# Kernel optimization log

Measured on AMD Instinct MI355X. Metric: run time of the kernel, lower is better.

The kernel has to match this reference:

```python
import jax, jax.numpy as jnp
import numpy as np

B = 32
NODES = [20480, 5120, 1280, 320, 80]
K = 6
Z = 64


def _cheb_sparse(x, src, dst, norm, W, b):
    # x: [B, N, F]; Chebyshev recursion with sparse normalized adjacency (edge list)
    def prop(t):
        return jnp.zeros_like(t).at[:, dst, :].add(t[:, src, :] * norm[None, :, None])
    Tx0 = x
    out = jnp.einsum('bnf,fo->bno', Tx0, W[0])
    Tx1 = prop(x)
    out = out + jnp.einsum('bnf,fo->bno', Tx1, W[1])
    for k in range(2, W.shape[0]):
        Tx2 = 2.0 * prop(Tx1) - Tx0
        out = out + jnp.einsum('bnf,fo->bno', Tx2, W[k])
        Tx0, Tx1 = Tx1, Tx2
    return out if b is None else out + b


def _cheb_dense(x, adj, W, b):
    # x: [B, N, F]; adj: dense [N, N] (adjacency_matrices[i].to_dense())
    Tx0 = x
    out = jnp.einsum('bnf,fo->bno', Tx0, W[0])
    Tx1 = jnp.einsum('mn,bnf->bmf', adj, x)
    out = out + jnp.einsum('bnf,fo->bno', Tx1, W[1])
    for k in range(2, W.shape[0]):
        Tx2 = 2.0 * jnp.einsum('mn,bnf->bmf', adj, Tx1) - Tx0
        out = out + jnp.einsum('bnf,fo->bno', Tx2, W[k])
        Tx0, Tx1 = Tx1, Tx2
    return out if b is None else out + b


def _pool(x, idx, w):
    # sparse pooling matrix with <=3 nnz/row: out[b,m,f] = sum_k w[m,k] * x[b, idx[m,k], f]
    return jnp.einsum('mk,bmkf->bmf', w, x[:, idx, :])


def setup_inputs() -> dict:
    key = jax.random.key(0)
    ks = iter(jax.random.split(key, 96))
    N0 = NODES[0]
    E = N0 * 6
    inp = {}
    inp['x'] = jax.random.normal(next(ks), (B * N0, 3), jnp.float32)
    ei = jax.random.randint(next(ks), (2, E), 0, N0, jnp.int32)
    inp['edge_index0'] = ei
    src, dst = ei[0], ei[1]
    deg = jnp.zeros((N0,), jnp.float32).at[src].add(1.0)
    dinv = jnp.where(deg > 0, deg ** -0.5, 0.0)
    inp['A_norm0'] = dinv[src] * dinv[dst]
    inp['batch_size'] = B
    for i in (1, 2, 3):
        n = NODES[i]
        inp[f'adj{i}'] = jax.random.uniform(next(ks), (n, n), jnp.float32) / n
    for i in range(4):
        m, n = NODES[i + 1], NODES[i]
        inp[f'down_idx{i}'] = jax.random.randint(next(ks), (m, 3), 0, n, jnp.int32)
        inp[f'down_w{i}'] = jax.random.uniform(next(ks), (m, 3), jnp.float32) / 3.0
        inp[f'up_idx{i}'] = jax.random.randint(next(ks), (n, 3), 0, m, jnp.int32)
        inp[f'up_w{i}'] = jax.random.uniform(next(ks), (n, 3), jnp.float32) / 3.0
    enc_io = [(3, 16), (16, 16), (16, 16), (16, 32)]
    for i, (fi, fo) in enumerate(enc_io):
        inp[f'W_enc{i}'] = 0.1 * jax.random.normal(next(ks), (K, fi, fo), jnp.float32)
        inp[f'b_enc{i}'] = 0.1 * jax.random.normal(next(ks), (fo,), jnp.float32)
    dec_io = [(32, 16), (16, 16), (16, 16), (16, 16), (16, 3)]
    for i, (fi, fo) in enumerate(dec_io):
        inp[f'W_dec{i}'] = 0.1 * jax.random.normal(next(ks), (K, fi, fo), jnp.float32)
        if i < 4:
            inp[f'b_dec{i}'] = 0.1 * jax.random.normal(next(ks), (fo,), jnp.float32)
    lat_in = NODES[4] * 32  # 2560
    inp['enc_w'] = 0.1 * jax.random.normal(next(ks), (Z, lat_in), jnp.float32)
    inp['enc_b'] = 0.1 * jax.random.normal(next(ks), (Z,), jnp.float32)
    inp['dec_w'] = 0.1 * jax.random.normal(next(ks), (lat_in, Z), jnp.float32)
    inp['dec_b'] = 0.1 * jax.random.normal(next(ks), (lat_in,), jnp.float32)
    return inp


def reference(x, edge_index0, A_norm0, batch_size, adj1, adj2, adj3,
              down_idx0, down_w0, up_idx0, up_w0, down_idx1, down_w1, up_idx1, up_w1,
              down_idx2, down_w2, up_idx2, up_w2, down_idx3, down_w3, up_idx3, up_w3,
              W_enc0, b_enc0, W_enc1, b_enc1, W_enc2, b_enc2, W_enc3, b_enc3,
              W_dec0, b_dec0, W_dec1, b_dec1, W_dec2, b_dec2, W_dec3, b_dec3, W_dec4,
              enc_w, enc_b, dec_w, dec_b):
    relu = jax.nn.relu
    src, dst = edge_index0[0], edge_index0[1]
    h = x.reshape(batch_size, -1, x.shape[-1])
    # encoder
    h = relu(_cheb_sparse(h, src, dst, A_norm0, W_enc0, b_enc0)); h = _pool(h, down_idx0, down_w0)
    h = relu(_cheb_dense(h, adj1, W_enc1, b_enc1)); h = _pool(h, down_idx1, down_w1)
    h = relu(_cheb_dense(h, adj2, W_enc2, b_enc2)); h = _pool(h, down_idx2, down_w2)
    h = relu(_cheb_dense(h, adj3, W_enc3, b_enc3)); h = _pool(h, down_idx3, down_w3)
    z = relu(h.reshape(batch_size, -1) @ enc_w.T + enc_b)
    # decoder
    h = relu(z @ dec_w.T + dec_b).reshape(batch_size, -1, W_dec0.shape[1])
    h = _pool(h, up_idx3, up_w3); h = relu(_cheb_dense(h, adj3, W_dec0, b_dec0))
    h = _pool(h, up_idx2, up_w2); h = relu(_cheb_dense(h, adj2, W_dec1, b_dec1))
    h = _pool(h, up_idx1, up_w1); h = relu(_cheb_dense(h, adj1, W_dec2, b_dec2))
    h = _pool(h, up_idx0, up_w0); h = relu(_cheb_sparse(h, src, dst, A_norm0, W_dec3, b_dec3))
    h = _cheb_sparse(h, src, dst, A_norm0, W_dec4, None)  # final layer, bias=None
    return h.reshape(-1, x.shape[-1])
```

## Files before the change

kernel.cpp:

```cpp
#include <hip/hip_runtime.h>

#define BATCH 32
#define NN0   20480

typedef __attribute__((ext_vector_type(8))) short short8v;
typedef __attribute__((ext_vector_type(4))) float f32x4;

__device__ __forceinline__ float bf2f(unsigned short h) {
    return __uint_as_float(((unsigned int)h) << 16);
}
__device__ __forceinline__ unsigned short f2bf(float x) {
    unsigned int u = __float_as_uint(x);
    u += 0x7fff + ((u >> 16) & 1);
    return (unsigned short)(u >> 16);
}
__device__ __forceinline__ unsigned int pk2(float a, float b) {
    return (unsigned int)f2bf(a) | ((unsigned int)f2bf(b) << 16);
}

__global__ __launch_bounds__(256) void count_kernel(const int* __restrict__ dst, int* __restrict__ cnt, int E) {
    int e = blockIdx.x * 256 + threadIdx.x;
    if (e < E) atomicAdd(&cnt[dst[e]], 1);
}

__global__ __launch_bounds__(256) void scan_kernel(const int* __restrict__ cnt, int* __restrict__ rowptr,
                                                   int* __restrict__ cursor, int n) {
    __shared__ int part[256];
    int tid = threadIdx.x;
    int per = (n + 255) / 256;
    int start = tid * per;
    int end = start + per; if (end > n) end = n; if (start > n) start = n;
    int s = 0;
    for (int i = start; i < end; ++i) s += cnt[i];
    part[tid] = s;
    __syncthreads();
    for (int off = 1; off < 256; off <<= 1) {
        int v = (tid >= off) ? part[tid - off] : 0;
        __syncthreads();
        part[tid] += v;
        __syncthreads();
    }
    int base = (tid == 0) ? 0 : part[tid - 1];
    for (int i = start; i < end; ++i) {
        rowptr[i] = base; cursor[i] = base;
        base += cnt[i];
    }
    if (tid == 255) rowptr[n] = base;
}

__global__ __launch_bounds__(256) void scatter_kernel(const int* __restrict__ src, const int* __restrict__ dst,
                                                      const float* __restrict__ nrm, int* __restrict__ cursor,
                                                      int* __restrict__ esrc, float* __restrict__ ewt,
                                                      int* __restrict__ eid, int E) {
    int e = blockIdx.x * 256 + threadIdx.x;
    if (e >= E) return;
    int p = atomicAdd(&cursor[dst[e]], 1);
    esrc[p] = src[e]; ewt[p] = nrm[e]; eid[p] = e;
}

__global__ __launch_bounds__(256) void sortrows_kernel(const int* __restrict__ rowptr, int* __restrict__ esrc,
                                                       float* __restrict__ ewt, int* __restrict__ eid, int N) {
    int m = blockIdx.x * 256 + threadIdx.x;
    if (m >= N) return;
    int a = rowptr[m], b = rowptr[m + 1];
    for (int i = a + 1; i < b; ++i) {
        int ke = eid[i]; int ks = esrc[i]; float kw = ewt[i];
        int j = i - 1;
        while (j >= a && eid[j] > ke) { eid[j+1]=eid[j]; esrc[j+1]=esrc[j]; ewt[j+1]=ewt[j]; --j; }
        eid[j+1] = ke; esrc[j+1] = ks; ewt[j+1] = kw;
    }
}

__global__ __launch_bounds__(256) void convert_flat(const float* __restrict__ in, unsigned short* __restrict__ out,
                                                    size_t n4) {
    for (size_t i = blockIdx.x * 256 + threadIdx.x; i < n4; i += (size_t)gridDim.x * 256) {
        float4 v = reinterpret_cast<const float4*>(in)[i];
        ushort4 o;
        o.x = f2bf(v.x); o.y = f2bf(v.y); o.z = f2bf(v.z); o.w = f2bf(v.w);
        reinterpret_cast<ushort4*>(out)[i] = o;
    }
}

__global__ __launch_bounds__(256) void xcopy_T(const float* __restrict__ x, unsigned short* __restrict__ out) {
    __shared__ unsigned short sh[32 * 96];
    const int m0 = blockIdx.x * 32;
    const int tid = threadIdx.x;
    const int b = tid >> 3, mi = tid & 7;
#pragma unroll
    for (int ii = 0; ii < 4; ++ii) {
        int mm = mi + ii * 8;
        const float* p = x + ((size_t)b * NN0 + m0 + mm) * 3;
        sh[mm * 96 + b * 3 + 0] = f2bf(p[0]);
        sh[mm * 96 + b * 3 + 1] = f2bf(p[1]);
        sh[mm * 96 + b * 3 + 2] = f2bf(p[2]);
    }
    __syncthreads();
    unsigned int* dst = (unsigned int*)(out + (size_t)m0 * 96);
    const unsigned int* srcp = (const unsigned int*)sh;
    for (int i = tid; i < 32 * 48; i += 256) dst[i] = srcp[i];
}

__global__ __launch_bounds__(256) void sparse_prop16(const int* __restrict__ rowptr, const int* __restrict__ esrc,
                                                     const float* __restrict__ ewt,
                                                     const unsigned short* __restrict__ Tin,
                                                     const unsigned short* __restrict__ Tprev,
                                                     unsigned short* __restrict__ Tout, float s, float t) {
    int g = blockIdx.x * 256 + threadIdx.x;
    int m = g >> 6, lane = g & 63;
    int e0 = rowptr[m], e1 = rowptr[m + 1];
    float acc[8] = {};
    for (int e = e0; e < e1; ++e) {
        float w = ewt[e];
        short8v v = *reinterpret_cast<const short8v*>(Tin + (size_t)esrc[e] * 512 + lane * 8);
#pragma unroll
        for (int j = 0; j < 8; ++j) acc[j] += w * bf2f((unsigned short)v[j]);
    }
    float r[8];
    if (Tprev) {
        short8v pv = *reinterpret_cast<const short8v*>(Tprev + (size_t)m * 512 + lane * 8);
#pragma unroll
        for (int j = 0; j < 8; ++j) r[j] = s * acc[j] + t * bf2f((unsigned short)pv[j]);
    } else {
#pragma unroll
        for (int j = 0; j < 8; ++j) r[j] = s * acc[j];
    }
    uint4 ov;
    ov.x = pk2(r[0], r[1]); ov.y = pk2(r[2], r[3]); ov.z = pk2(r[4], r[5]); ov.w = pk2(r[6], r[7]);
    *reinterpret_cast<uint4*>(Tout + (size_t)m * 512 + lane * 8) = ov;
}

__global__ __launch_bounds__(256) void sparse_prop3(const int* __restrict__ rowptr, const int* __restrict__ esrc,
                                                    const float* __restrict__ ewt,
                                                    const unsigned short* __restrict__ Tin,
                                                    const unsigned short* __restrict__ Tprev,
                                                    unsigned short* __restrict__ Tout, float s, float t) {
    int g = blockIdx.x * 256 + threadIdx.x;
    int m = g / 96, c = g - m * 96;
    int e0 = rowptr[m], e1 = rowptr[m + 1];
    float acc = 0.f;
    for (int e = e0; e < e1; ++e)
        acc += ewt[e] * bf2f(Tin[(size_t)esrc[e] * 96 + c]);
    float v = s * acc;
    if (Tprev) v += t * bf2f(Tprev[(size_t)m * 96 + c]);
    Tout[(size_t)m * 96 + c] = f2bf(v);
}

template <int FIN, int FOUT>
__global__ __launch_bounds__(256) void sparse_epi(const unsigned short* __restrict__ S, size_t slot,
                                                  const float* __restrict__ W, const float* __restrict__ bias,
                                                  unsigned short* __restrict__ out, int relu) {
    __shared__ float Ws[6 * FIN * FOUT];
    for (int i = threadIdx.x; i < 6 * FIN * FOUT; i += 256) Ws[i] = W[i];
    __syncthreads();
    int g = blockIdx.x * 256 + threadIdx.x;
    int m = g >> 5, b = g & 31;
    float oa[FOUT];
#pragma unroll
    for (int o = 0; o < FOUT; ++o) oa[o] = bias ? bias[o] : 0.f;
    for (int k = 0; k < 6; ++k) {
        const unsigned short* p = S + (size_t)k * slot + (size_t)m * (32 * FIN) + b * FIN;
        float xv[FIN];
        if constexpr (FIN == 16) {
            short8v v0 = *reinterpret_cast<const short8v*>(p);
            short8v v1 = *reinterpret_cast<const short8v*>(p + 8);
#pragma unroll
            for (int f = 0; f < 8; ++f) { xv[f] = bf2f((unsigned short)v0[f]); xv[f + 8] = bf2f((unsigned short)v1[f]); }
        } else {
#pragma unroll
            for (int f = 0; f < FIN; ++f) xv[f] = bf2f(p[f]);
        }
#pragma unroll
        for (int f = 0; f < FIN; ++f)
#pragma unroll
            for (int o = 0; o < FOUT; ++o) oa[o] += xv[f] * Ws[(k * FIN + f) * FOUT + o];
    }
    unsigned short* orow = out + (size_t)m * (32 * FOUT) + b * FOUT;
    unsigned int u[FOUT / 2];
#pragma unroll
    for (int o = 0; o < FOUT / 2; ++o) {
        float a = oa[2 * o], c = oa[2 * o + 1];
        if (relu) { a = fmaxf(a, 0.f); c = fmaxf(c, 0.f); }
        u[o] = pk2(a, c);
    }
#pragma unroll
    for (int q = 0; q < FOUT / 8; ++q)
        reinterpret_cast<uint4*>(orow)[q] = make_uint4(u[4 * q], u[4 * q + 1], u[4 * q + 2], u[4 * q + 3]);
}

__global__ __launch_bounds__(256) void sparse_epi_final(const unsigned short* __restrict__ S, size_t slot,
                                                        const float* __restrict__ W, float* __restrict__ dout) {
    __shared__ float Ws[6 * 16 * 3];
    __shared__ float sh[32 * 24];
    for (int i = threadIdx.x; i < 288; i += 256) Ws[i] = W[i];
    __syncthreads();
    const int tid = threadIdx.x;
    const int mm = tid >> 5, b = tid & 31;
    const int m = blockIdx.x * 8 + mm;
    float o0 = 0.f, o1 = 0.f, o2 = 0.f;
    for (int k = 0; k < 6; ++k) {
        const unsigned short* p = S + (size_t)k * slot + (size_t)m * 512 + b * 16;
        short8v v0 = *reinterpret_cast<const short8v*>(p);
        short8v v1 = *reinterpret_cast<const short8v*>(p + 8);
#pragma unroll
        for (int f = 0; f < 16; ++f) {
            float xf = bf2f((unsigned short)(f < 8 ? v0[f] : v1[f - 8]));
            o0 += xf * Ws[(k * 16 + f) * 3 + 0];
            o1 += xf * Ws[(k * 16 + f) * 3 + 1];
            o2 += xf * Ws[(k * 16 + f) * 3 + 2];
        }
    }
    sh[b * 24 + mm * 3 + 0] = o0;
    sh[b * 24 + mm * 3 + 1] = o1;
    sh[b * 24 + mm * 3 + 2] = o2;
    __syncthreads();
    const size_t base = (size_t)blockIdx.x * 24;
    for (int i = tid; i < 768; i += 256) {
        int b2 = i / 24, r = i - b2 * 24;
        dout[(size_t)b2 * (NN0 * 3) + base + r] = sh[i];
    }
}

__device__ __forceinline__ float ldv(const float* p) { return *p; }
__device__ __forceinline__ float ldv(const unsigned short* p) { return bf2f(*p); }

template <typename TI>
__global__ __launch_bounds__(256) void pool_cT(const TI* __restrict__ in, const int* __restrict__ idx,
                                               const float* __restrict__ w, unsigned short* __restrict__ out,
                                               int C, int Mnew) {
    __shared__ float tile[32][33];
    const int m0 = blockIdx.x * 32, c0 = blockIdx.y * 32;
    const int tx = threadIdx.x & 31, ty = threadIdx.x >> 5;
#pragma unroll
    for (int i = 0; i < 4; ++i) {
        int mn = m0 + ty + i * 8;
        const int* ir = idx + mn * 3; const float* wr = w + mn * 3;
        float v = wr[0] * ldv(in + (size_t)ir[0] * C + c0 + tx)
                + wr[1] * ldv(in + (size_t)ir[1] * C + c0 + tx)
                + wr[2] * ldv(in + (size_t)ir[2] * C + c0 + tx);
        tile[ty + i * 8][tx] = v;
    }
    __syncthreads();
#pragma unroll
    for (int i = 0; i < 4; ++i) {
        int c = c0 + ty + i * 8;
        out[(size_t)c * Mnew + m0 + tx] = f2bf(tile[tx][ty + i * 8]);
    }
}

__global__ __launch_bounds__(256) void pool_row16(const unsigned short* __restrict__ in, const int* __restrict__ idx,
                                                  const float* __restrict__ w, unsigned short* __restrict__ out) {
    int g = blockIdx.x * 256 + threadIdx.x;
    int m = g >> 6, lane = g & 63;
    const int* ir = idx + m * 3; const float* wr = w + m * 3;
    short8v a = *reinterpret_cast<const short8v*>(in + (size_t)ir[0] * 512 + lane * 8);
    short8v b = *reinterpret_cast<const short8v*>(in + (size_t)ir[1] * 512 + lane * 8);
    short8v c = *reinterpret_cast<const short8v*>(in + (size_t)ir[2] * 512 + lane * 8);
    float r[8];
#pragma unroll
    for (int j = 0; j < 8; ++j)
        r[j] = wr[0] * bf2f((unsigned short)a[j]) + wr[1] * bf2f((unsigned short)b[j]) + wr[2] * bf2f((unsigned short)c[j]);
    uint4 ov;
    ov.x = pk2(r[0], r[1]); ov.y = pk2(r[2], r[3]); ov.z = pk2(r[4], r[5]); ov.w = pk2(r[6], r[7]);
    *reinterpret_cast<uint4*>(out + (size_t)m * 512 + lane * 8) = ov;
}

__global__ __launch_bounds__(256) void pool_f32(const unsigned short* __restrict__ in, const int* __restrict__ idx,
                                                const float* __restrict__ w, float* __restrict__ out) {
    int g = blockIdx.x * 256 + threadIdx.x;
    int m = g >> 10, c = g & 1023;
    const int* ir = idx + m * 3; const float* wr = w + m * 3;
    out[g] = wr[0] * bf2f(in[(size_t)ir[0] * 1024 + c])
           + wr[1] * bf2f(in[(size_t)ir[1] * 1024 + c])
           + wr[2] * bf2f(in[(size_t)ir[2] * 1024 + c]);
}

template <int MF, bool SPLIT>
__global__ __launch_bounds__(256) void gemm_mfma(const unsigned short* __restrict__ Ab,
                                                 const unsigned short* __restrict__ Xb,
                                                 const unsigned short* __restrict__ Pb,
                                                 unsigned short* __restrict__ Ob,
                                                 float* __restrict__ Pf,
                                                 int Mn, int KC, float s, float t) {
    constexpr int BM = MF * 64;
    __shared__ unsigned short As[BM * 64];
    __shared__ unsigned short Xs[64 * 64];
    const int tid = threadIdx.x;
    const int lane = tid & 63, wid = tid >> 6;
    int lin = blockIdx.y * gridDim.x + blockIdx.x;
    int nwg = gridDim.x * gridDim.y;
    int lin2 = (lin & 7) * (nwg >> 3) + (lin >> 3);
    int by = lin2 / gridDim.x, bx = lin2 - by * gridDim.x;
    const int bm = by * BM, bc = bx * 64;
    const int kbase = SPLIT ? blockIdx.z * KC : 0;

    f32x4 acc[MF][4] = {};
    constexpr int SEGA = (BM * 64 * 2) / 1024 / 4;

    for (int k0 = kbase; k0 < kbase + KC; k0 += 64) {
        __syncthreads();
#pragma unroll
        for (int i = 0; i < SEGA; ++i) {
            int o = (wid * SEGA + i) * 1024 + lane * 16;
            int row = o >> 7;
            int colb = (o & 127) ^ ((row & 7) << 4);
            const unsigned short* g = Ab + (size_t)(bm + row) * Mn + k0 + (colb >> 1);
            __builtin_amdgcn_global_load_lds((const __attribute__((address_space(1))) void*)g,
                                             (__attribute__((address_space(3))) void*)((char*)As + (size_t)(wid * SEGA + i) * 1024),
                                             16, 0, 0);
        }
#pragma unroll
        for (int i = 0; i < 2; ++i) {
            int o = (wid * 2 + i) * 1024 + lane * 16;
            int row = o >> 7;
            int colb = (o & 127) ^ ((row & 7) << 4);
            const unsigned short* g = Xb + (size_t)(bc + row) * Mn + k0 + (colb >> 1);
            __builtin_amdgcn_global_load_lds((const __attribute__((address_space(1))) void*)g,
                                             (__attribute__((address_space(3))) void*)((char*)Xs + (size_t)(wid * 2 + i) * 1024),
                                             16, 0, 0);
        }
        __syncthreads();
#pragma unroll
        for (int kk = 0; kk < 2; ++kk) {
            short8v a[MF], b[4];
#pragma unroll
            for (int mf = 0; mf < MF; ++mf) {
                int r = wid * (MF * 16) + mf * 16 + (lane & 15);
                int cb = kk * 64 + ((lane >> 4) * 16);
                int addr = r * 128 + (cb ^ ((r & 7) << 4));
                a[mf] = *reinterpret_cast<const short8v*>((const char*)As + addr);
            }
#pragma unroll
            for (int cf = 0; cf < 4; ++cf) {
                int r = cf * 16 + (lane & 15);
                int cb = kk * 64 + ((lane >> 4) * 16);
                int addr = r * 128 + (cb ^ ((r & 7) << 4));
                b[cf] = *reinterpret_cast<const short8v*>((const char*)Xs + addr);
            }
#pragma unroll
            for (int mf = 0; mf < MF; ++mf)
#pragma unroll
                for (int cf = 0; cf < 4; ++cf)
                    acc[mf][cf] = __builtin_amdgcn_mfma_f32_16x16x32_bf16(a[mf], b[cf], acc[mf][cf], 0, 0, 0);
        }
    }
#pragma unroll
    for (int mf = 0; mf < MF; ++mf) {
        int m0 = bm + wid * (MF * 16) + mf * 16 + ((lane >> 4) * 4);
#pragma unroll
        for (int cf = 0; cf < 4; ++cf) {
            int c = bc + cf * 16 + (lane & 15);
            size_t base = (size_t)c * Mn + m0;
            if constexpr (SPLIT) {
                size_t zbase = (size_t)blockIdx.z * (size_t)(gridDim.x * 64) * (size_t)Mn;
                *reinterpret_cast<float4*>(Pf + zbase + base) =
                    make_float4(acc[mf][cf][0], acc[mf][cf][1], acc[mf][cf][2], acc[mf][cf][3]);
            } else {
                float v0 = s * acc[mf][cf][0], v1 = s * acc[mf][cf][1];
                float v2 = s * acc[mf][cf][2], v3 = s * acc[mf][cf][3];
                if (Pb) {
                    uint2 pv = *reinterpret_cast<const uint2*>(Pb + base);
                    v0 += t * bf2f((unsigned short)(pv.x & 0xffff));
                    v1 += t * bf2f((unsigned short)(pv.x >> 16));
                    v2 += t * bf2f((unsigned short)(pv.y & 0xffff));
                    v3 += t * bf2f((unsigned short)(pv.y >> 16));
                }
                uint2 ov;
                ov.x = pk2(v0, v1); ov.y = pk2(v2, v3);
                *reinterpret_cast<uint2*>(Ob + base) = ov;
            }
        }
    }
}

__global__ __launch_bounds__(256) void sk_reduce(const float* __restrict__ Pf,
                                                 const unsigned short* __restrict__ Prev,
                                                 unsigned short* __restrict__ Out,
                                                 int n4, int KS, float s, float t) {
    int g = blockIdx.x * 256 + threadIdx.x;
    if (g >= n4) return;
    float4 a = reinterpret_cast<const float4*>(Pf)[g];
    for (int ks = 1; ks < KS; ++ks) {
        float4 b = reinterpret_cast<const float4*>(Pf)[(size_t)ks * n4 + g];
        a.x += b.x; a.y += b.y; a.z += b.z; a.w += b.w;
    }
    float v0 = s * a.x, v1 = s * a.y, v2 = s * a.z, v3 = s * a.w;
    if (Prev) {
        uint2 pv = reinterpret_cast<const uint2*>(Prev)[g];
        v0 += t * bf2f((unsigned short)(pv.x & 0xffff));
        v1 += t * bf2f((unsigned short)(pv.x >> 16));
        v2 += t * bf2f((unsigned short)(pv.y & 0xffff));
        v3 += t * bf2f((unsigned short)(pv.y >> 16));
    }
    uint2 ov;
    ov.x = pk2(v0, v1); ov.y = pk2(v2, v3);
    reinterpret_cast<uint2*>(Out)[g] = ov;
}

template <int FIN, int FOUT>
__global__ __launch_bounds__(256) void epi_layer(const unsigned short* __restrict__ Tb, size_t tslot,
                                                 const float* __restrict__ W, const float* __restrict__ bias,
                                                 unsigned short* __restrict__ out, int M) {
    __shared__ float Ws[6 * FIN * FOUT];
    for (int i = threadIdx.x; i < 6 * FIN * FOUT; i += 256) Ws[i] = W[i];
    __syncthreads();
    int g = blockIdx.x * 256 + threadIdx.x;
    int b = g / M, m = g - b * M;
    float oa[FOUT];
#pragma unroll
    for (int o = 0; o < FOUT; ++o) oa[o] = bias[o];
    for (int k = 0; k < 6; ++k) {
        const unsigned short* Tk = Tb + (size_t)k * tslot + (size_t)b * FIN * M + m;
#pragma unroll
        for (int f = 0; f < FIN; ++f) {
            float xf = bf2f(Tk[(size_t)f * M]);
#pragma unroll
            for (int o = 0; o < FOUT; ++o) oa[o] += xf * Ws[(k * FIN + f) * FOUT + o];
        }
    }
    unsigned short* orow = out + (size_t)m * (32 * FOUT) + b * FOUT;
    unsigned int u[FOUT / 2];
#pragma unroll
    for (int o = 0; o < FOUT / 2; ++o)
        u[o] = pk2(fmaxf(oa[2 * o], 0.f), fmaxf(oa[2 * o + 1], 0.f));
#pragma unroll
    for (int q = 0; q < FOUT / 8; ++q)
        reinterpret_cast<uint4*>(orow)[q] = make_uint4(u[4 * q], u[4 * q + 1], u[4 * q + 2], u[4 * q + 3]);
}

__global__ __launch_bounds__(256) void fc_enc_kernel(const float* __restrict__ h, const float* __restrict__ w,
                                                     const float* __restrict__ bias, float* __restrict__ z) {
    __shared__ float sh[256];
    int b = blockIdx.x, o = threadIdx.x & 63, q = threadIdx.x >> 6;
    float acc = 0.f;
    for (int n = q * 20; n < q * 20 + 20; ++n)
#pragma unroll
        for (int f = 0; f < 32; ++f)
            acc += h[((size_t)n * 32 + b) * 32 + f] * w[(size_t)o * 2560 + n * 32 + f];
    sh[threadIdx.x] = acc;
    __syncthreads();
    if (q == 0) z[b * 64 + o] = fmaxf(sh[o] + sh[64 + o] + sh[128 + o] + sh[192 + o] + bias[o], 0.f);
}

__global__ __launch_bounds__(256) void fc_dec_kernel(const float* __restrict__ z, const float* __restrict__ w,
                                                     const float* __restrict__ bias, float* __restrict__ out) {
    int g = blockIdx.x * 256 + threadIdx.x;
    if (g >= 80 * 32 * 32) return;
    int f = g % 32; int b = (g / 32) % 32; int n = g / 1024;
    int j = n * 32 + f;
    float acc = bias[j];
    const float* wr = w + (size_t)j * 64;
    const float* zr = z + b * 64;
#pragma unroll
    for (int o = 0; o < 64; ++o) acc += zr[o] * wr[o];
    out[g] = fmaxf(acc, 0.f);
}

extern "C" void kernel_launch(void* const* d_in, const int* in_sizes, int n_in,
                              void* d_out, int out_size, void* d_ws, size_t ws_size,
                              hipStream_t stream) {
    (void)n_in; (void)out_size; (void)ws_size;
    const float* x     = (const float*)d_in[0];
    const int*   ei    = (const int*)d_in[1];
    const float* anorm = (const float*)d_in[2];
    const float* adjs[3] = { (const float*)d_in[4], (const float*)d_in[5], (const float*)d_in[6] };
    const int*   dn_idx[4] = { (const int*)d_in[7],  (const int*)d_in[11], (const int*)d_in[15], (const int*)d_in[19] };
    const float* dn_w[4]   = { (const float*)d_in[8],(const float*)d_in[12],(const float*)d_in[16],(const float*)d_in[20] };
    const int*   up_idx[4] = { (const int*)d_in[9],  (const int*)d_in[13], (const int*)d_in[17], (const int*)d_in[21] };
    const float* up_w[4]   = { (const float*)d_in[10],(const float*)d_in[14],(const float*)d_in[18],(const float*)d_in[22] };
    const float* W_enc[4] = { (const float*)d_in[23], (const float*)d_in[25], (const float*)d_in[27], (const float*)d_in[29] };
    const float* b_enc[4] = { (const float*)d_in[24], (const float*)d_in[26], (const float*)d_in[28], (const float*)d_in[30] };
    const float* W_dec[5] = { (const float*)d_in[31], (const float*)d_in[33], (const float*)d_in[35], (const float*)d_in[37], (const float*)d_in[39] };
    const float* b_dec[4] = { (const float*)d_in[32], (const float*)d_in[34], (const float*)d_in[36], (const float*)d_in[38] };
    const float* enc_w = (const float*)d_in[40];
    const float* enc_b = (const float*)d_in[41];
    const float* dec_w = (const float*)d_in[42];
    const float* dec_b = (const float*)d_in[43];
    const int E = in_sizes[2];

    const size_t SLOT16 = (size_t)NN0 * 512;
    const size_t SLOT3  = (size_t)NN0 * 96;
    unsigned short* S = (unsigned short*)d_ws;
    float* Pf = (float*)d_ws;
    unsigned short* Tb = S + 3 * SLOT16;
    unsigned short* HB = Tb + (size_t)6 * 512 * 5120;
    char* p = (char*)(HB + SLOT16);
    unsigned short* adj1b = (unsigned short*)p; p += (size_t)5120 * 5120 * 2;
    unsigned short* adj2b = (unsigned short*)p; p += (size_t)1280 * 1280 * 2;
    unsigned short* adj3b = (unsigned short*)p; p += (size_t)320 * 320 * 2;
    int* rowptr = (int*)p;  p += (NN0 + 4) * sizeof(int);
    int* cnt    = (int*)p;  p += NN0 * sizeof(int);
    int* cursor = (int*)p;  p += NN0 * sizeof(int);
    int* esrc   = (int*)p;  p += (size_t)E * sizeof(int);
    int* eid    = (int*)p;  p += (size_t)E * sizeof(int);
    float* ewt  = (float*)p; p += (size_t)E * sizeof(float);
    float* lat0 = (float*)p; p += 80 * 1024 * sizeof(float);
    float* zb   = (float*)p; p += 32 * 64 * sizeof(float);
    float* lat1 = (float*)p;

    hipMemsetAsync(cnt, 0, NN0 * sizeof(int), stream);
    count_kernel<<<(E + 255) / 256, 256, 0, stream>>>(ei + E, cnt, E);
    scan_kernel<<<1, 256, 0, stream>>>(cnt, rowptr, cursor, NN0);
    scatter_kernel<<<(E + 255) / 256, 256, 0, stream>>>(ei, ei + E, anorm, cursor, esrc, ewt, eid, E);
    sortrows_kernel<<<(NN0 + 255) / 256, 256, 0, stream>>>(rowptr, esrc, ewt, eid, NN0);

    convert_flat<<<2048, 256, 0, stream>>>(adjs[0], adj1b, (size_t)5120 * 5120 / 4);
    convert_flat<<<512, 256, 0, stream>>>(adjs[1], adj2b, (size_t)1280 * 1280 / 4);
    convert_flat<<<64, 256, 0, stream>>>(adjs[2], adj3b, (size_t)320 * 320 / 4);

    auto dense_layer = [&](const unsigned short* Ab, int M, int FIN, int FOUT,
                           const float* W, const float* bias, unsigned short* HBout) {
        const int C = 32 * FIN;
        const size_t tslot = (size_t)C * M;
        const int CM4 = (int)(tslot / 4);
        int KS, KC, BMv, MFv;
        if (M == 5120)      { BMv = 128; MFv = 2; KS = 4; KC = 1280; }
        else if (M == 1280) { BMv = 64;  MFv = 1; KS = 4; KC = 320;  }
        else                { BMv = 64;  MFv = 1; KS = 1; KC = M;    }
        dim3 gg(C / 64, M / BMv, KS);
        for (int k = 1; k < 6; ++k) {
            const unsigned short* Xin = Tb + (size_t)(k - 1) * tslot;
            const unsigned short* Pv  = (k >= 2) ? Tb + (size_t)(k - 2) * tslot : nullptr;
            unsigned short* Oo = Tb + (size_t)k * tslot;
            float s = (k == 1) ? 1.f : 2.f;
            float t = (k == 1) ? 0.f : -1.f;
            if (KS > 1) {
                if (MFv == 2) gemm_mfma<2, true><<<gg, 256, 0, stream>>>(Ab, Xin, nullptr, nullptr, Pf, M, KC, s, t);
                else          gemm_mfma<1, true><<<gg, 256, 0, stream>>>(Ab, Xin, nullptr, nullptr, Pf, M, KC, s, t);
                sk_reduce<<<(CM4 + 255) / 256, 256, 0, stream>>>(Pf, Pv, Oo, CM4, KS, s, t);
            } else {
                gemm_mfma<1, false><<<gg, 256, 0, stream>>>(Ab, Xin, Pv, Oo, nullptr, M, KC, s, t);
            }
        }
        int blocks = M * 32 / 256;
        if (FIN == 16 && FOUT == 16)      epi_layer<16, 16><<<blocks, 256, 0, stream>>>(Tb, tslot, W, bias, HBout, M);
        else if (FIN == 16 && FOUT == 32) epi_layer<16, 32><<<blocks, 256, 0, stream>>>(Tb, tslot, W, bias, HBout, M);
        else                              epi_layer<32, 16><<<blocks, 256, 0, stream>>>(Tb, tslot, W, bias, HBout, M);
    };
    auto sparse_layer16 = [&](const float* W, const float* bias, int final_relu, unsigned short* out16) {
        for (int k = 1; k < 6; ++k) {
            const unsigned short* Tin = S + (size_t)(k - 1) * SLOT16;
            const unsigned short* Pv  = (k >= 2) ? S + (size_t)(k - 2) * SLOT16 : nullptr;
            sparse_prop16<<<NN0 / 4, 256, 0, stream>>>(rowptr, esrc, ewt, Tin, Pv, S + (size_t)k * SLOT16,
                                                       (k == 1) ? 1.f : 2.f, (k == 1) ? 0.f : -1.f);
        }
        if (out16) sparse_epi<16, 16><<<NN0 * 32 / 256, 256, 0, stream>>>(S, SLOT16, W, bias, out16, final_relu);
        else       sparse_epi_final<<<NN0 / 8, 256, 0, stream>>>(S, SLOT16, W, (float*)d_out);
    };

    xcopy_T<<<NN0 / 32, 256, 0, stream>>>(x, S);
    for (int k = 1; k < 6; ++k) {
        const unsigned short* Tin = S + (size_t)(k - 1) * SLOT3;
        const unsigned short* Pv  = (k >= 2) ? S + (size_t)(k - 2) * SLOT3 : nullptr;
        sparse_prop3<<<NN0 * 96 / 256, 256, 0, stream>>>(rowptr, esrc, ewt, Tin, Pv, S + (size_t)k * SLOT3,
                                                         (k == 1) ? 1.f : 2.f, (k == 1) ? 0.f : -1.f);
    }
    sparse_epi<3, 16><<<NN0 * 32 / 256, 256, 0, stream>>>(S, SLOT3, W_enc[0], b_enc[0], HB, 1);
    { dim3 g(5120 / 32, 512 / 32);  pool_cT<unsigned short><<<g, 256, 0, stream>>>(HB, dn_idx[0], dn_w[0], Tb, 512, 5120); }
    dense_layer(adj1b, 5120, 16, 16, W_enc[1], b_enc[1], HB);
    { dim3 g(1280 / 32, 512 / 32);  pool_cT<unsigned short><<<g, 256, 0, stream>>>(HB, dn_idx[1], dn_w[1], Tb, 512, 1280); }
    dense_layer(adj2b, 1280, 16, 16, W_enc[2], b_enc[2], HB);
    { dim3 g(320 / 32, 512 / 32);   pool_cT<unsigned short><<<g, 256, 0, stream>>>(HB, dn_idx[2], dn_w[2], Tb, 512, 320); }
    dense_layer(adj3b, 320, 16, 32, W_enc[3], b_enc[3], HB);
    pool_f32<<<80 * 1024 / 256, 256, 0, stream>>>(HB, dn_idx[3], dn_w[3], lat0);
    fc_enc_kernel<<<32, 256, 0, stream>>>(lat0, enc_w, enc_b, zb);
    fc_dec_kernel<<<80 * 32 * 32 / 256, 256, 0, stream>>>(zb, dec_w, dec_b, lat1);
    { dim3 g(320 / 32, 1024 / 32);  pool_cT<float><<<g, 256, 0, stream>>>(lat1, up_idx[3], up_w[3], Tb, 1024, 320); }
    dense_layer(adj3b, 320, 32, 16, W_dec[0], b_dec[0], HB);
    { dim3 g(1280 / 32, 512 / 32);  pool_cT<unsigned short><<<g, 256, 0, stream>>>(HB, up_idx[2], up_w[2], Tb, 512, 1280); }
    dense_layer(adj2b, 1280, 16, 16, W_dec[1], b_dec[1], HB);
    { dim3 g(5120 / 32, 512 / 32);  pool_cT<unsigned short><<<g, 256, 0, stream>>>(HB, up_idx[1], up_w[1], Tb, 512, 5120); }
    dense_layer(adj1b, 5120, 16, 16, W_dec[2], b_dec[2], HB);
    pool_row16<<<NN0 / 4, 256, 0, stream>>>(HB, up_idx[0], up_w[0], S);
    sparse_layer16(W_dec[3], b_dec[3], 1, S);
    sparse_layer16(W_dec[4], nullptr, 0, nullptr);
}
```

Baseline: 1.542 ms.

## Double-buffer LDS tiles in MFMA GEMM and halve split-K for large layer

The GEMM kernel now keeps two LDS buffers for the A and X tiles. It issues the global-to-LDS loads for the next K tile before computing on the current one, with one barrier per iteration instead of two, and precomputes the per-thread source addresses. The aim is to hide global load latency behind the MFMA work. The M=5120 layer also drops split-K from 4 to 2 with a larger K chunk, which halves the partial-sum traffic to the reduce kernel but leaves fewer workgroups. Doubling LDS may lower occupancy.

Measured after the change: 1.482 ms. 3.9% less time.

```diff
diff --git a/kernel.cpp b/kernel.cpp
--- a/kernel.cpp
+++ b/kernel.cpp
@@ -282,8 +282,11 @@
                                                  float* __restrict__ Pf,
                                                  int Mn, int KC, float s, float t) {
     constexpr int BM = MF * 64;
-    __shared__ unsigned short As[BM * 64];
-    __shared__ unsigned short Xs[64 * 64];
+    constexpr int ABYTES = BM * 64 * 2;
+    constexpr int XBYTES = 64 * 64 * 2;
+    constexpr int SEGA = ABYTES / 1024 / 4;
+    __shared__ unsigned short As[2][BM * 64];
+    __shared__ unsigned short Xs[2][64 * 64];
     const int tid = threadIdx.x;
     const int lane = tid & 63, wid = tid >> 6;
     int lin = blockIdx.y * gridDim.x + blockIdx.x;
@@ -292,33 +295,51 @@
     int by = lin2 / gridDim.x, bx = lin2 - by * gridDim.x;
     const int bm = by * BM, bc = bx * 64;
     const int kbase = SPLIT ? blockIdx.z * KC : 0;
+    const int NT = KC / 64;
+
+    const unsigned short* gAsrc[SEGA];
+    unsigned int ldsAoff[SEGA];
+#pragma unroll
+    for (int i = 0; i < SEGA; ++i) {
+        int o = (wid * SEGA + i) * 1024 + lane * 16;
+        int row = o >> 7;
+        int colb = (o & 127) ^ ((row & 7) << 4);
+        gAsrc[i] = Ab + (size_t)(bm + row) * Mn + kbase + (colb >> 1);
+        ldsAoff[i] = (unsigned int)(wid * SEGA + i) * 1024;
+    }
+    const unsigned short* gXsrc[2];
+    unsigned int ldsXoff[2];
+#pragma unroll
+    for (int i = 0; i < 2; ++i) {
+        int o = (wid * 2 + i) * 1024 + lane * 16;
+        int row = o >> 7;
+        int colb = (o & 127) ^ ((row & 7) << 4);
+        gXsrc[i] = Xb + (size_t)(bc + row) * Mn + kbase + (colb >> 1);
+        ldsXoff[i] = (unsigned int)(wid * 2 + i) * 1024;
+    }
+
+    auto STAGE = [&](int buf, int ko) {
+#pragma unroll
+        for (int i = 0; i < SEGA; ++i)
+            __builtin_amdgcn_global_load_lds((const __attribute__((address_space(1))) void*)(gAsrc[i] + ko),
+                                             (__attribute__((address_space(3))) void*)((char*)As + buf * ABYTES + ldsAoff[i]),
+                                             16, 0, 0);
+#pragma unroll
+        for (int i = 0; i < 2; ++i)
+            __builtin_amdgcn_global_load_lds((const __attribute__((address_space(1))) void*)(gXsrc[i] + ko),
+                                             (__attribute__((address_space(3))) void*)((char*)Xs + buf * XBYTES + ldsXoff[i]),
+                                             16, 0, 0);
+    };
 
     f32x4 acc[MF][4] = {};
-    constexpr int SEGA = (BM * 64 * 2) / 1024 / 4;
-
-    for (int k0 = kbase; k0 < kbase + KC; k0 += 64) {
-        __syncthreads();
-#pragma unroll
-        for (int i = 0; i < SEGA; ++i) {
-            int o = (wid * SEGA + i) * 1024 + lane * 16;
-            int row = o >> 7;
-            int colb = (o & 127) ^ ((row & 7) << 4);
-            const unsigned short* g = Ab + (size_t)(bm + row) * Mn + k0 + (colb >> 1);
-            __builtin_amdgcn_global_load_lds((const __attribute__((address_space(1))) void*)g,
-                                             (__attribute__((address_space(3))) void*)((char*)As + (size_t)(wid * SEGA + i) * 1024),
-                                             16, 0, 0);
-        }
-#pragma unroll
-        for (int i = 0; i < 2; ++i) {
-            int o = (wid * 2 + i) * 1024 + lane * 16;
-            int row = o >> 7;
-            int colb = (o & 127) ^ ((row & 7) << 4);
-            const unsigned short* g = Xb + (size_t)(bc + row) * Mn + k0 + (colb >> 1);
-            __builtin_amdgcn_global_load_lds((const __attribute__((address_space(1))) void*)g,
-                                             (__attribute__((address_space(3))) void*)((char*)Xs + (size_t)(wid * 2 + i) * 1024),
-                                             16, 0, 0);
-        }
-        __syncthreads();
+
+    STAGE(0, 0);
+    __syncthreads();
+    for (int tt = 0; tt < NT; ++tt) {
+        const int cur = tt & 1;
+        if (tt + 1 < NT) STAGE(cur ^ 1, (tt + 1) * 64);
+        const char* Ac = (const char*)As + cur * ABYTES;
+        const char* Xc = (const char*)Xs + cur * XBYTES;
 #pragma unroll
         for (int kk = 0; kk < 2; ++kk) {
             short8v a[MF], b[4];
@@ -327,14 +348,14 @@
                 int r = wid * (MF * 16) + mf * 16 + (lane & 15);
                 int cb = kk * 64 + ((lane >> 4) * 16);
                 int addr = r * 128 + (cb ^ ((r & 7) << 4));
-                a[mf] = *reinterpret_cast<const short8v*>((const char*)As + addr);
+                a[mf] = *reinterpret_cast<const short8v*>(Ac + addr);
             }
 #pragma unroll
             for (int cf = 0; cf < 4; ++cf) {
                 int r = cf * 16 + (lane & 15);
                 int cb = kk * 64 + ((lane >> 4) * 16);
                 int addr = r * 128 + (cb ^ ((r & 7) << 4));
-                b[cf] = *reinterpret_cast<const short8v*>((const char*)Xs + addr);
+                b[cf] = *reinterpret_cast<const short8v*>(Xc + addr);
             }
 #pragma unroll
             for (int mf = 0; mf < MF; ++mf)
@@ -342,7 +363,9 @@
                 for (int cf = 0; cf < 4; ++cf)
                     acc[mf][cf] = __builtin_amdgcn_mfma_f32_16x16x32_bf16(a[mf], b[cf], acc[mf][cf], 0, 0, 0);
         }
-    }
+        __syncthreads();
+    }
+
 #pragma unroll
     for (int mf = 0; mf < MF; ++mf) {
         int m0 = bm + wid * (MF * 16) + mf * 16 + ((lane >> 4) * 4);
@@ -513,7 +536,7 @@
         const size_t tslot = (size_t)C * M;
         const int CM4 = (int)(tslot / 4);
         int KS, KC, BMv, MFv;
-        if (M == 5120)      { BMv = 128; MFv = 2; KS = 4; KC = 1280; }
+        if (M == 5120)      { BMv = 128; MFv = 2; KS = 2; KC = 2560; }
         else if (M == 1280) { BMv = 64;  MFv = 1; KS = 4; KC = 320;  }
         else                { BMv = 64;  MFv = 1; KS = 1; KC = M;    }
         dim3 gg(C / 64, M / BMv, KS);
```
